# Kernel tuning notes

Hardware: AMD Instinct MI355X
Metric: run time of the kernel (lower is better)

The kernel has to match this reference:

```python
import jax, jax.numpy as jnp
import numpy as np

NUM_HEADS = 8

def conv1x1(w, x, b=None):
    # w: [O, C], x: [B, C, H, W] -> [B, O, H, W]
    y = jnp.einsum('oc,bchw->bohw', w, x)
    if b is not None:
        y = y + b[None, :, None, None]
    return y

def setup_inputs() -> dict:
    key = jax.random.key(0)
    ks = jax.random.split(key, 8)
    B, C, H, W = 8, 512, 32, 32
    s = lambda fan: 1.0 / np.sqrt(fan)
    return {
        'x': jax.random.normal(ks[0], (B, C, H, W), jnp.float32),
        'W_qkv': jax.random.normal(ks[1], (3 * C, C), jnp.float32) * s(C),
        'W_proj': jax.random.normal(ks[2], (C, C), jnp.float32) * s(C),
        'b_proj': jax.random.normal(ks[3], (C,), jnp.float32) * 0.01,
        'W_att1': jax.random.normal(ks[4], (C // 4, C), jnp.float32) * s(C),
        'b_att1': jax.random.normal(ks[5], (C // 4,), jnp.float32) * 0.01,
        'W_att2': jax.random.normal(ks[6], (1, C // 4), jnp.float32) * s(C // 4),
        'b_att2': jax.random.normal(ks[7], (1,), jnp.float32) * 0.01,
    }

def reference(x, W_qkv, W_proj, b_proj, W_att1, b_att1, W_att2, b_att2):
    B, C, H, W = x.shape
    nh = NUM_HEADS
    dh = C // nh
    N = H * W
    qkv = conv1x1(W_qkv, x)                      # [B, 3C, H, W]
    qkv = qkv.reshape(B, 3, nh, dh, N)
    qkv = jnp.transpose(qkv, (1, 0, 2, 4, 3))    # [3, B, nh, N, dh]
    q, k, v = qkv[0], qkv[1], qkv[2]
    attn = jnp.einsum('bhnd,bhmd->bhnm', q, k) * (dh ** -0.5)
    attn = jax.nn.softmax(attn, axis=-1)         # dropout is identity at eval
    o = jnp.einsum('bhnm,bhmd->bhnd', attn, v)   # [B, nh, N, dh]
    # Faithful to torch: transpose(1,2) then raw reshape to (B, C, H, W)
    o = jnp.swapaxes(o, 1, 2).reshape(B, C, H, W)
    out = conv1x1(W_proj, o, b_proj)             # [B, C, H, W]
    h1 = jax.nn.relu(conv1x1(W_att1, out, b_att1))
    spatial_att = jax.nn.sigmoid(conv1x1(W_att2, h1, b_att2))  # [B, 1, H, W]
    out = out * spatial_att
    return (out, spatial_att)
```

## Files before the change

kernel.cpp:

```cpp
#include <hip/hip_runtime.h>
#include <hip/hip_bf16.h>

using bf16 = __hip_bfloat16;
typedef __bf16 bf16x8 __attribute__((ext_vector_type(8)));
typedef float  f32x4  __attribute__((ext_vector_type(4)));


static constexpr int B  = 8;
static constexpr int C  = 512;
static constexpr int N  = 1024;
static constexpr int NH = 8;
static constexpr int DH = 64;
static constexpr int CQ = 128;

static constexpr float QSCALE = 0.125f * 1.44269504f;

static constexpr size_t QKV_OFF  = 0;
static constexpr size_t H1_OFF   = 25165824;

__device__ __forceinline__ unsigned pack2(float lo, float hi) {
  __hip_bfloat162 h = __float22bfloat162_rn(make_float2(lo, hi));
  return *(unsigned*)&h;
}
__device__ __forceinline__ int swz(int row, int col) {
  return row * 64 + ((((col >> 3) ^ row) & 7) << 3) + (col & 7);
}
__device__ __forceinline__ bf16x8 ldfrag(const short* tl, int row, int kk, int lane) {
  const int atom = 4 * kk + (lane >> 4);
  return *(const bf16x8*)&tl[row * 64 + (((atom ^ row) & 7) << 3)];
}
__device__ __forceinline__ bf16x8 ldfragF(const short* tl, int row, int kk, int lane) {
  const int atom = 4 * kk + (lane >> 4);
  return *(const bf16x8*)&tl[row * 64 + (((atom ^ row ^ (row >> 2)) & 7) << 3)];
}
__device__ __forceinline__ int fswz(int row, int col) {
  return row * 64 + ((((col >> 2) ^ row) & 15) << 2) + (col & 3);
}

__global__ __launch_bounds__(256, 3) void k_qkv(const float* __restrict__ W,
                                                const float* __restrict__ x,
                                                bf16* __restrict__ qkv) {
  __shared__ __align__(16) short Al[128 * 64];
  __shared__ __align__(16) short Bl[128 * 64];
  const int pt = blockIdx.x, ot = blockIdx.y, b = blockIdx.z;
  const int p0 = pt * 128, o0 = ot * 128;
  const int t = threadIdx.x, l = t & 63, w = t >> 6;
  const int wo = w & 1, wp = w >> 1;
  const int g = t >> 5, k32 = t & 31;
  const int r16 = t >> 4, q16 = t & 15;
  const float* xsrc = x + ((size_t)b * C + 8 * g) * N + p0 + 4 * k32;
  const float* wsrc = W + (size_t)(o0 + r16) * C + 4 * q16;
  unsigned upx[16], upw[16];
  auto ld = [&](int kc) {
    const float* xa = xsrc + (size_t)kc * N;
#pragma unroll
    for (int u = 0; u < 4; ++u) {
      float4 r0 = *(const float4*)(xa + (size_t)(2 * u) * N);
      float4 r1 = *(const float4*)(xa + (size_t)(2 * u + 1) * N);
      upx[4*u+0] = pack2(r0.x, r1.x);
      upx[4*u+1] = pack2(r0.y, r1.y);
      upx[4*u+2] = pack2(r0.z, r1.z);
      upx[4*u+3] = pack2(r0.w, r1.w);
    }
    const float* wa = wsrc + kc;
#pragma unroll
    for (int i = 0; i < 8; ++i) {
      float4 f = *(const float4*)(wa + (size_t)(16 * i) * C);
      upw[2*i]   = pack2(f.x, f.y);
      upw[2*i+1] = pack2(f.z, f.w);
    }
  };
  f32x4 acc[4][4] = {};
  ld(0);
  for (int kc = 0; kc < C; kc += 64) {
    __syncthreads();
#pragma unroll
    for (int j = 0; j < 4; ++j) {
      const int p = 4 * k32 + j;
      uint4 v = make_uint4(upx[j], upx[4 + j], upx[8 + j], upx[12 + j]);
      *(uint4*)&Al[p * 64 + (((g ^ p ^ (p >> 2)) & 7) << 3)] = v;
    }
#pragma unroll
    for (int i = 0; i < 8; ++i) {
      const int R = 16 * i + r16;
      *(uint2*)&Bl[R * 64 + ((((q16 >> 1) ^ R) & 7) << 3) + 4 * (q16 & 1)] =
          make_uint2(upw[2 * i], upw[2 * i + 1]);
    }
    __syncthreads();
    if (kc + 64 < C) ld(kc + 64);
#pragma unroll
    for (int kk = 0; kk < 2; ++kk) {
      bf16x8 af[4], bf[4];
#pragma unroll
      for (int i = 0; i < 4; ++i) af[i] = ldfrag(Bl, wo*64 + i*16 + (l&15), kk, l);
#pragma unroll
      for (int j = 0; j < 4; ++j) bf[j] = ldfragF(Al, wp*64 + j*16 + (l&15), kk, l);
#pragma unroll
      for (int i = 0; i < 4; ++i)
#pragma unroll
        for (int j = 0; j < 4; ++j)
          acc[i][j] = __builtin_amdgcn_mfma_f32_16x16x32_bf16(af[i], bf[j], acc[i][j], 0, 0, 0);
    }
  }
  const float qs = (ot < 4) ? QSCALE : 1.0f;
  __syncthreads();
  {
    short* T = wo ? Bl : Al;
#pragma unroll
    for (int i = 0; i < 4; ++i) {
      const int d = i * 16 + 4 * (l >> 4);
#pragma unroll
      for (int j = 0; j < 4; ++j) {
        const int p = wp * 64 + j * 16 + (l & 15);
        *(unsigned*)&T[swz(p, d)]     = pack2(acc[i][j][0] * qs, acc[i][j][1] * qs);
        *(unsigned*)&T[swz(p, d + 2)] = pack2(acc[i][j][2] * qs, acc[i][j][3] * qs);
      }
    }
  }
  __syncthreads();
  {
    const int oc0 = o0, oc1 = o0 + 64;
    bf16* dst0 = qkv + (size_t)(oc0 >> 9) * (B * NH * N * DH) +
                 (size_t)(b * NH + ((oc0 >> 6) & 7)) * N * DH + (size_t)p0 * DH;
    bf16* dst1 = qkv + (size_t)(oc1 >> 9) * (B * NH * N * DH) +
                 (size_t)(b * NH + ((oc1 >> 6) & 7)) * N * DH + (size_t)p0 * DH;
#pragma unroll
    for (int it = 0; it < 8; ++it) {
      const int e = t + 256 * it;
      const int tile = e >> 10, row = (e >> 3) & 127, atom = e & 7;
      const short* T = tile ? Bl : Al;
      uint4 val = *(const uint4*)&T[row * 64 + (((atom ^ row) & 7) << 3)];
      bf16* dst = tile ? dst1 : dst0;
      *(uint4*)(dst + (size_t)row * DH + atom * 8) = val;
    }
  }
}

__global__ __launch_bounds__(256) void k_attn(bf16* __restrict__ qkv) {
  __shared__ __align__(16) short Sh[20480];
  const int bh = blockIdx.x, qt = blockIdx.y;
  const int t = threadIdx.x, l = t & 63, w = t >> 6;
  const bf16* kp = qkv + (size_t)B * NH * N * DH;
  const bf16* vp = kp + (size_t)B * NH * N * DH;
  const uint4* gkb = (const uint4*)(kp + (size_t)bh * N * DH);
  const uint4* gvb = (const uint4*)(vp + (size_t)bh * N * DH);
  const int kpr = t & 31, g = t >> 5;
  short* Pw = Sh + 16384 + w * 1024;

  uint4 kreg0, kreg1, v0, v1;
  auto ld = [&](int mt) {
    const uint4* gk = gkb + mt * 512;
    kreg0 = gk[t]; kreg1 = gk[t + 256];
    const uint4* gv = gvb + mt * 512;
    v0 = gv[16 * kpr + g]; v1 = gv[16 * kpr + 8 + g];
  };
  auto stage = [&](short* Kn, short* Vn) {
    const int r0 = t >> 3, a0 = t & 7;
    *(uint4*)&Kn[r0 * 64 + (((a0 ^ r0) & 7) << 3)] = kreg0;
    const int r1 = r0 + 32;
    *(uint4*)&Kn[r1 * 64 + (((a0 ^ r1) & 7) << 3)] = kreg1;
    const unsigned* v0d = (const unsigned*)&v0;
    const unsigned* v1d = (const unsigned*)&v1;
#pragma unroll
    for (int j = 0; j < 8; ++j) {
      unsigned pk = __builtin_amdgcn_perm(v1d[j >> 1], v0d[j >> 1],
                                          (j & 1) ? 0x07060302u : 0x05040100u);
      *(unsigned*)&Vn[swz(g * 8 + j, 2 * kpr)] = pk;
    }
  };

  {
    const uint4* gq = (const uint4*)(qkv + ((size_t)bh * N + qt * 64) * DH);
    for (int c = t; c < 512; c += 256) {
      int row = c >> 3, atom = c & 7;
      *(uint4*)&Sh[row * 64 + (((atom ^ row) & 7) << 3)] = gq[c];
    }
  }
  ld(0);
  __syncthreads();
  bf16x8 qf[2] = { ldfrag(Sh, w * 16 + (l & 15), 0, l),
                   ldfrag(Sh, w * 16 + (l & 15), 1, l) };
  stage(Sh + 4096, Sh + 8192);
  ld(1);
  __syncthreads();

  bf16x8 onesf;
#pragma unroll
  for (int i = 0; i < 8; ++i) onesf[i] = (__bf16)1.0f;
  f32x4 oacc[4] = {};
  f32x4 lacc = {};

  for (int mt = 0; mt < 16; ++mt) {
    const int cur = mt & 1;
    const short* Kc = Sh + (cur ? 0 : 4096);
    const short* Vc = Sh + (cur ? 12288 : 8192);
    f32x4 sacc[4] = {};
#pragma unroll
    for (int kk = 0; kk < 2; ++kk)
#pragma unroll
      for (int kt = 0; kt < 4; ++kt) {
        bf16x8 af = ldfrag(Kc, kt * 16 + (l & 15), kk, l);
        sacc[kt] = __builtin_amdgcn_mfma_f32_16x16x32_bf16(af, qf[kk], sacc[kt], 0, 0, 0);
      }
    const int qr = l & 15, cb0 = 4 * (l >> 4);
#pragma unroll
    for (int kt = 0; kt < 4; ++kt) {
      float p0v = __builtin_exp2f(sacc[kt][0]);
      float p1v = __builtin_exp2f(sacc[kt][1]);
      float p2v = __builtin_exp2f(sacc[kt][2]);
      float p3v = __builtin_exp2f(sacc[kt][3]);
      const int cb = kt * 16 + cb0;
      *(unsigned*)&Pw[swz(qr, cb)]     = pack2(p0v, p1v);
      *(unsigned*)&Pw[swz(qr, cb + 2)] = pack2(p2v, p3v);
    }
#pragma unroll
    for (int kk = 0; kk < 2; ++kk) {
      bf16x8 pbf = ldfrag(Pw, l & 15, kk, l);
      lacc = __builtin_amdgcn_mfma_f32_16x16x32_bf16(onesf, pbf, lacc, 0, 0, 0);
#pragma unroll
      for (int dt = 0; dt < 4; ++dt) {
        bf16x8 av = ldfrag(Vc, dt * 16 + (l & 15), kk, l);
        oacc[dt] = __builtin_amdgcn_mfma_f32_16x16x32_bf16(av, pbf, oacc[dt], 0, 0, 0);
      }
    }
    if (mt < 15) {
      short* Kn = Sh + (cur ? 4096 : 0);
      short* Vn = Sh + (cur ? 8192 : 12288);
      stage(Kn, Vn);
      if (mt < 14) ld(mt + 2);
      __syncthreads();
    }
  }
  __syncthreads();
  const float inv = 1.f / lacc[0];
  const int qr = l & 15, cb0 = 4 * (l >> 4);
#pragma unroll
  for (int dt = 0; dt < 4; ++dt) {
    const int cb = dt * 16 + cb0;
    *(unsigned*)&Pw[swz(qr, cb)]     = pack2(oacc[dt][0] * inv, oacc[dt][1] * inv);
    *(unsigned*)&Pw[swz(qr, cb + 2)] = pack2(oacc[dt][2] * inv, oacc[dt][3] * inv);
  }
  __syncthreads();
  bf16* obase = qkv + ((size_t)bh * N + qt * 64 + w * 16) * DH;
#pragma unroll
  for (int i = 0; i < 2; ++i) {
    const int e = l + 64 * i, row = e >> 3, atom = e & 7;
    uint4 val = *(const uint4*)&Pw[row * 64 + (((atom ^ row) & 7) << 3)];
    *(uint4*)(obase + (size_t)row * DH + atom * 8) = val;
  }
}

__global__ __launch_bounds__(256) void k_proj(const float* __restrict__ Wp,
                                              const float* __restrict__ bp,
                                              const bf16* __restrict__ obuf,
                                              float* __restrict__ outd) {
  __shared__ __align__(16) short SM[8192];
  short* Wl = SM;
  short* Ot = SM + 4096;
  const int pt = blockIdx.x, ct = blockIdx.y, b = blockIdx.z;
  const int p0 = pt * 64, co0 = ct * 64;
  const int h = (p0 & 511) >> 6, eps = p0 >> 9;
  const int t = threadIdx.x, l = t & 63, w = t >> 6;
  const int so = t & 63, sg = t >> 6;
  const int cp = t & 31, g = t >> 5;
  const float* wsrc = &Wp[(size_t)(co0 + so) * C + sg * 16];
  const bf16* obase = obuf + (size_t)(b * NH + h) * N * DH;
  union u4s { uint4 v; unsigned short s[8]; };
  float4 wreg[4]; u4s o0r, o1r;
  auto ld = [&](int kc) {
    const float4* wp_ = (const float4*)(wsrc + kc);
    wreg[0] = wp_[0]; wreg[1] = wp_[1]; wreg[2] = wp_[2]; wreg[3] = wp_[3];
    const int ci0 = kc + 2 * cp;
    o0r.v = *(const uint4*)(obase + (size_t)(2 * ci0 + eps) * 64 + g * 8);
    o1r.v = *(const uint4*)(obase + (size_t)(2 * ci0 + 2 + eps) * 64 + g * 8);
  };
  f32x4 acc[4] = {};
  ld(0);
  for (int kc = 0; kc < C; kc += 64) {
    __syncthreads();
#pragma unroll
    for (int u = 0; u < 4; ++u) {
      const int c0 = sg * 16 + 4 * u;
      *(unsigned*)&Wl[swz(so, c0)]     = pack2(wreg[u].x, wreg[u].y);
      *(unsigned*)&Wl[swz(so, c0 + 2)] = pack2(wreg[u].z, wreg[u].w);
    }
#pragma unroll
    for (int i = 0; i < 8; ++i)
      *(unsigned*)&Ot[swz(g * 8 + i, 2 * cp)] =
          (unsigned)o0r.s[i] | ((unsigned)o1r.s[i] << 16);
    __syncthreads();
    if (kc + 64 < C) ld(kc + 64);
    const int mrow = w * 16 + (l & 15);
#pragma unroll
    for (int kk = 0; kk < 2; ++kk) {
      bf16x8 a = ldfrag(Ot, mrow, kk, l);
#pragma unroll
      for (int nt = 0; nt < 4; ++nt) {
        bf16x8 bf = ldfrag(Wl, nt * 16 + (l & 15), kk, l);
        acc[nt] = __builtin_amdgcn_mfma_f32_16x16x32_bf16(a, bf, acc[nt], 0, 0, 0);
      }
    }
  }
  __syncthreads();
  {
    float* Ep = (float*)SM;
    const int pp = w * 16 + 4 * (l >> 4);
#pragma unroll
    for (int nt = 0; nt < 4; ++nt) {
      const int co = nt * 16 + (l & 15);
      const float bias = bp[co0 + co];
      *(float2*)&Ep[fswz(co, pp)]     = make_float2(acc[nt][0] + bias, acc[nt][1] + bias);
      *(float2*)&Ep[fswz(co, pp + 2)] = make_float2(acc[nt][2] + bias, acc[nt][3] + bias);
    }
  }
  __syncthreads();
  {
    const float* Ep = (const float*)SM;
#pragma unroll
    for (int it = 0; it < 4; ++it) {
      const int e = t + 256 * it;
      const int co = e >> 4, a = e & 15;
      float4 v = *(const float4*)&Ep[co * 64 + (((a ^ (co & 15)) & 15) << 2)];
      *(float4*)&outd[(size_t)b * C * N + (size_t)(co0 + co) * N + p0 + a * 4] = v;
    }
  }
}

__global__ __launch_bounds__(256) void k_att1(const float* __restrict__ W1,
                                              const float* __restrict__ b1,
                                              const float* __restrict__ outd,
                                              bf16* __restrict__ h1b) {
  __shared__ __align__(16) short Wl[64 * 64];
  __shared__ __align__(16) short Xt[64 * 64];
  const int pt = blockIdx.x, jt = blockIdx.y, b = blockIdx.z;
  const int p0 = pt * 64, j0 = jt * 64;
  const int t = threadIdx.x, l = t & 63, w = t >> 6;
  const int so = t & 63, sg = t >> 6;
  const int cp = t & 31, g = t >> 5;
  const float* wsrc = &W1[(size_t)(j0 + so) * C + sg * 16];
  const float* xsrc = &outd[((size_t)b * C + 2 * cp) * N + p0 + g * 8];
  float4 wreg[4], xreg[4];
  auto ld = [&](int kc) {
    const float4* wp_ = (const float4*)(wsrc + kc);
    wreg[0] = wp_[0]; wreg[1] = wp_[1]; wreg[2] = wp_[2]; wreg[3] = wp_[3];
    const float4* x0_ = (const float4*)(xsrc + (size_t)kc * N);
    xreg[0] = x0_[0]; xreg[1] = x0_[1];
    const float4* x1_ = (const float4*)(xsrc + (size_t)(kc + 1) * N);
    xreg[2] = x1_[0]; xreg[3] = x1_[1];
  };
  f32x4 acc[4] = {};
  ld(0);
  for (int kc = 0; kc < C; kc += 64) {
    __syncthreads();
#pragma unroll
    for (int u = 0; u < 4; ++u) {
      const int c0 = sg * 16 + 4 * u;
      *(unsigned*)&Wl[swz(so, c0)]     = pack2(wreg[u].x, wreg[u].y);
      *(unsigned*)&Wl[swz(so, c0 + 2)] = pack2(wreg[u].z, wreg[u].w);
    }
    {
      float a0[8], a1[8];
      *(float4*)&a0[0] = xreg[0]; *(float4*)&a0[4] = xreg[1];
      *(float4*)&a1[0] = xreg[2]; *(float4*)&a1[4] = xreg[3];
#pragma unroll
      for (int i = 0; i < 8; ++i)
        *(unsigned*)&Xt[swz(g * 8 + i, 2 * cp)] = pack2(a0[i], a1[i]);
    }
    __syncthreads();
    if (kc + 64 < C) ld(kc + 64);
    const int mrow = w * 16 + (l & 15);
#pragma unroll
    for (int kk = 0; kk < 2; ++kk) {
      bf16x8 a = ldfrag(Xt, mrow, kk, l);
#pragma unroll
      for (int nt = 0; nt < 4; ++nt) {
        bf16x8 bf = ldfrag(Wl, nt * 16 + (l & 15), kk, l);
        acc[nt] = __builtin_amdgcn_mfma_f32_16x16x32_bf16(a, bf, acc[nt], 0, 0, 0);
      }
    }
  }
  __syncthreads();
  {
    const int pp = w * 16 + 4 * (l >> 4);
#pragma unroll
    for (int nt = 0; nt < 4; ++nt) {
      const int jo = nt * 16 + (l & 15);
      const float bias = b1[j0 + jo];
      float v0 = fmaxf(acc[nt][0] + bias, 0.f), v1 = fmaxf(acc[nt][1] + bias, 0.f);
      float v2 = fmaxf(acc[nt][2] + bias, 0.f), v3 = fmaxf(acc[nt][3] + bias, 0.f);
      *(unsigned*)&Wl[swz(jo, pp)]     = pack2(v0, v1);
      *(unsigned*)&Wl[swz(jo, pp + 2)] = pack2(v2, v3);
    }
  }
  __syncthreads();
#pragma unroll
  for (int it = 0; it < 2; ++it) {
    const int e = t + 256 * it;
    const int row = e >> 3, atom = e & 7;
    uint4 val = *(const uint4*)&Wl[row * 64 + (((atom ^ row) & 7) << 3)];
    *(uint4*)((bf16*)h1b + (size_t)b * CQ * N + (size_t)(j0 + row) * N + p0 + atom * 8) = val;
  }
}

__global__ __launch_bounds__(256) void k_gate(const float* __restrict__ W2,
                                              const float* __restrict__ b2,
                                              const bf16* __restrict__ h1b,
                                              float* __restrict__ out0,
                                              float* __restrict__ out1) {
  __shared__ float red[8][32];
  __shared__ __align__(16) float att[32];
  const int blk = blockIdx.x, t = threadIdx.x;
  const int b = blk >> 5, p0 = (blk & 31) * 32;
  const int pl = t & 31, jg = t >> 5;
  float acc = 0.f;
  const bf16* hb = h1b + ((size_t)b * CQ + jg * 16) * N + p0 + pl;
#pragma unroll
  for (int jj = 0; jj < 16; ++jj)
    acc += W2[jg * 16 + jj] * __bfloat162float(hb[(size_t)jj * N]);
  red[jg][pl] = acc;
  __syncthreads();
  if (t < 32) {
    float a = b2[0];
#pragma unroll
    for (int k = 0; k < 8; ++k) a += red[k][t];
    const float sg = 1.f / (1.f + __expf(-a));
    att[t] = sg;
    out1[b * N + p0 + t] = sg;
  }
  __syncthreads();
  const int p4 = t & 7, cc = t >> 3;
  float4* ob4 = (float4*)(out0 + (size_t)b * C * N + p0);
  const float4 sg4 = *(const float4*)&att[4 * p4];
  for (int c = cc; c < C; c += 32) {
    float4 v = ob4[c * 256 + p4];
    v.x *= sg4.x; v.y *= sg4.y; v.z *= sg4.z; v.w *= sg4.w;
    ob4[c * 256 + p4] = v;
  }
}

extern "C" void kernel_launch(void* const* d_in, const int* in_sizes, int n_in,
                              void* d_out, int out_size, void* d_ws, size_t ws_size,
                              hipStream_t stream) {
  const float* x     = (const float*)d_in[0];
  const float* Wqkv  = (const float*)d_in[1];
  const float* Wproj = (const float*)d_in[2];
  const float* bproj = (const float*)d_in[3];
  const float* Watt1 = (const float*)d_in[4];
  const float* batt1 = (const float*)d_in[5];
  const float* Watt2 = (const float*)d_in[6];
  const float* batt2 = (const float*)d_in[7];

  char* ws = (char*)d_ws;
  bf16* qkvb = (bf16*)(ws + QKV_OFF);
  bf16* h1b  = (bf16*)(ws + H1_OFF);

  float* out0 = (float*)d_out;
  float* out1 = out0 + (size_t)B * C * N;

  k_qkv <<<dim3(8, 12, 8), 256, 0, stream>>>(Wqkv, x, qkvb);
  k_attn<<<dim3(64, 16),   256, 0, stream>>>(qkvb);
  k_proj<<<dim3(16, 8, 8), 256, 0, stream>>>(Wproj, bproj, qkvb, out0);
  k_att1<<<dim3(16, 2, 8), 256, 0, stream>>>(Watt1, batt1, out0, h1b);
  k_gate<<<256, 256, 0, stream>>>(Watt2, batt2, h1b, out0, out1);
}
```

Before: 193.0 us.

## Load K fragments directly from global and single-buffer V in LDS for attention

The attention kernel no longer stages K tiles through shared memory. Each wave now loads its K MFMA fragments straight from global memory into registers, and V becomes a single LDS buffer instead of a double buffer. LDS use falls from 40KB to 16KB and launch bounds request 4 blocks per CU, aiming at higher occupancy. The costs are redundant global K reads across the four waves, a synchronisation that now stalls on V staging every iteration, and the removal of the barrier before the final output readback.

Result: slower. 227.5 us (+17.8%).

```diff
diff --git a/kernel.cpp b/kernel.cpp
--- a/kernel.cpp
+++ b/kernel.cpp
@@ -136,36 +136,29 @@
   }
 }
 
-__global__ __launch_bounds__(256) void k_attn(bf16* __restrict__ qkv) {
-  __shared__ __align__(16) short Sh[20480];
+__global__ __launch_bounds__(256, 4) void k_attn(bf16* __restrict__ qkv) {
+  __shared__ __align__(16) short Sh[8192];
   const int bh = blockIdx.x, qt = blockIdx.y;
   const int t = threadIdx.x, l = t & 63, w = t >> 6;
-  const bf16* kp = qkv + (size_t)B * NH * N * DH;
+  const bf16* kp = qkv + (size_t)B * NH * N * DH + (size_t)bh * N * DH;
   const bf16* vp = kp + (size_t)B * NH * N * DH;
-  const uint4* gkb = (const uint4*)(kp + (size_t)bh * N * DH);
-  const uint4* gvb = (const uint4*)(vp + (size_t)bh * N * DH);
   const int kpr = t & 31, g = t >> 5;
-  short* Pw = Sh + 16384 + w * 1024;
-
-  uint4 kreg0, kreg1, v0, v1;
-  auto ld = [&](int mt) {
-    const uint4* gk = gkb + mt * 512;
-    kreg0 = gk[t]; kreg1 = gk[t + 256];
-    const uint4* gv = gvb + mt * 512;
+  short* Vt = Sh;
+  short* Pw = Sh + 4096 + w * 1024;
+
+  uint4 v0, v1;
+  auto ldv = [&](int mt) {
+    const uint4* gv = (const uint4*)(vp + (size_t)mt * 64 * DH);
     v0 = gv[16 * kpr + g]; v1 = gv[16 * kpr + 8 + g];
   };
-  auto stage = [&](short* Kn, short* Vn) {
-    const int r0 = t >> 3, a0 = t & 7;
-    *(uint4*)&Kn[r0 * 64 + (((a0 ^ r0) & 7) << 3)] = kreg0;
-    const int r1 = r0 + 32;
-    *(uint4*)&Kn[r1 * 64 + (((a0 ^ r1) & 7) << 3)] = kreg1;
+  auto stageV = [&]() {
     const unsigned* v0d = (const unsigned*)&v0;
     const unsigned* v1d = (const unsigned*)&v1;
 #pragma unroll
     for (int j = 0; j < 8; ++j) {
       unsigned pk = __builtin_amdgcn_perm(v1d[j >> 1], v0d[j >> 1],
                                           (j & 1) ? 0x07060302u : 0x05040100u);
-      *(unsigned*)&Vn[swz(g * 8 + j, 2 * kpr)] = pk;
+      *(unsigned*)&Vt[swz(g * 8 + j, 2 * kpr)] = pk;
     }
   };
 
@@ -176,12 +169,10 @@
       *(uint4*)&Sh[row * 64 + (((atom ^ row) & 7) << 3)] = gq[c];
     }
   }
-  ld(0);
+  ldv(0);
   __syncthreads();
   bf16x8 qf[2] = { ldfrag(Sh, w * 16 + (l & 15), 0, l),
                    ldfrag(Sh, w * 16 + (l & 15), 1, l) };
-  stage(Sh + 4096, Sh + 8192);
-  ld(1);
   __syncthreads();
 
   bf16x8 onesf;
@@ -189,20 +180,25 @@
   for (int i = 0; i < 8; ++i) onesf[i] = (__bf16)1.0f;
   f32x4 oacc[4] = {};
   f32x4 lacc = {};
+  const int qr = l & 15, cb0 = 4 * (l >> 4);
 
   for (int mt = 0; mt < 16; ++mt) {
-    const int cur = mt & 1;
-    const short* Kc = Sh + (cur ? 0 : 4096);
-    const short* Vc = Sh + (cur ? 12288 : 8192);
+    bf16x8 kf[8];
+    const bf16* kt0 = kp + ((size_t)mt * 64 + (l & 15)) * DH + (l >> 4) * 8;
+#pragma unroll
+    for (int kk = 0; kk < 2; ++kk)
+#pragma unroll
+      for (int kt = 0; kt < 4; ++kt)
+        kf[4 * kk + kt] = *(const bf16x8*)(kt0 + kt * 16 * DH + kk * 32);
+    stageV();
+    __syncthreads();
+    if (mt < 15) ldv(mt + 1);
     f32x4 sacc[4] = {};
 #pragma unroll
     for (int kk = 0; kk < 2; ++kk)
 #pragma unroll
-      for (int kt = 0; kt < 4; ++kt) {
-        bf16x8 af = ldfrag(Kc, kt * 16 + (l & 15), kk, l);
-        sacc[kt] = __builtin_amdgcn_mfma_f32_16x16x32_bf16(af, qf[kk], sacc[kt], 0, 0, 0);
-      }
-    const int qr = l & 15, cb0 = 4 * (l >> 4);
+      for (int kt = 0; kt < 4; ++kt)
+        sacc[kt] = __builtin_amdgcn_mfma_f32_16x16x32_bf16(kf[4*kk+kt], qf[kk], sacc[kt], 0, 0, 0);
 #pragma unroll
     for (int kt = 0; kt < 4; ++kt) {
       float p0v = __builtin_exp2f(sacc[kt][0]);
@@ -219,28 +215,19 @@
       lacc = __builtin_amdgcn_mfma_f32_16x16x32_bf16(onesf, pbf, lacc, 0, 0, 0);
 #pragma unroll
       for (int dt = 0; dt < 4; ++dt) {
-        bf16x8 av = ldfrag(Vc, dt * 16 + (l & 15), kk, l);
+        bf16x8 av = ldfrag(Vt, dt * 16 + (l & 15), kk, l);
         oacc[dt] = __builtin_amdgcn_mfma_f32_16x16x32_bf16(av, pbf, oacc[dt], 0, 0, 0);
       }
     }
-    if (mt < 15) {
-      short* Kn = Sh + (cur ? 4096 : 0);
-      short* Vn = Sh + (cur ? 8192 : 12288);
-      stage(Kn, Vn);
-      if (mt < 14) ld(mt + 2);
-      __syncthreads();
-    }
-  }
-  __syncthreads();
+    if (mt < 15) __syncthreads();
+  }
   const float inv = 1.f / lacc[0];
-  const int qr = l & 15, cb0 = 4 * (l >> 4);
 #pragma unroll
   for (int dt = 0; dt < 4; ++dt) {
     const int cb = dt * 16 + cb0;
     *(unsigned*)&Pw[swz(qr, cb)]     = pack2(oacc[dt][0] * inv, oacc[dt][1] * inv);
     *(unsigned*)&Pw[swz(qr, cb + 2)] = pack2(oacc[dt][2] * inv, oacc[dt][3] * inv);
   }
-  __syncthreads();
   bf16* obase = qkv + ((size_t)bh * N + qt * 64 + w * 16) * DH;
 #pragma unroll
   for (int i = 0; i < 2; ++i) {
```
